# Kernel optimization log

Measured on AMD Instinct MI355X. Metric: run time of the kernel, lower is better.

The kernel has to match this reference:

```python
import jax, jax.numpy as jnp
import numpy as np

TAU = 2.0      # LIF membrane time constant
EPS = 1e-5     # BatchNorm eps
ALPHA = 4.0    # spikingjelly default Sigmoid surrogate alpha

@jax.custom_vjp
def spike(v):
    return (v >= 0.0).astype(v.dtype)

def _spike_fwd(v):
    return (v >= 0.0).astype(v.dtype), v

def _spike_bwd(v, g):
    s = jax.nn.sigmoid(ALPHA * v)
    return (g * ALPHA * s * (1.0 - s),)

spike.defvjp(_spike_fwd, _spike_bwd)

def lif(x_seq, v_th=1.0):
    # MultiStepLIFNode: v' = v + (x - v)/tau; spike = H(v' - v_th); hard reset to 0 (detach_reset)
    def step(v, x):
        v = v + (x - v) / TAU
        s = spike(v - v_th)
        v = v * (1.0 - jax.lax.stop_gradient(s))
        return v, s
    _, spikes = jax.lax.scan(step, jnp.zeros_like(x_seq[0]), x_seq)
    return spikes

def bn(y, gamma, beta, mean, var, trailing):
    # inference-mode BatchNorm over channel axis 2 of [T,B,C,...]
    shp = (1, 1, -1) + (1,) * trailing
    inv = gamma / jnp.sqrt(var + EPS)
    return (y - mean.reshape(shp)) * inv.reshape(shp) + beta.reshape(shp)

def setup_inputs() -> dict:
    T, B, C, H, W = 4, 32, 512, 16, 16
    key = jax.random.key(0)
    ks = jax.random.split(key, 12)
    return {
        "x": jax.random.normal(ks[0], (T, B, C, H, W), jnp.float32),
        "q_w": jax.random.normal(ks[1], (C, C), jnp.float32) * 0.02,
        "k_w": jax.random.normal(ks[2], (C, C), jnp.float32) * 0.02,
        "v_w": jax.random.normal(ks[3], (C, C), jnp.float32) * 0.02,
        "proj_w": jax.random.normal(ks[4], (C, C), jnp.float32) * 0.02,
        "proj_b": jax.random.normal(ks[5], (C,), jnp.float32) * 0.02,
        "dwc_w": jax.random.normal(ks[6], (C, 1, 5, 5), jnp.float32) * 0.1,
        "dwc_b": jax.random.normal(ks[7], (C,), jnp.float32) * 0.02,
        "bn_gamma": jax.random.uniform(ks[8], (5, C), jnp.float32, 0.5, 1.5),
        "bn_beta": jax.random.normal(ks[9], (5, C), jnp.float32) * 0.1,
        "bn_mean": jax.random.normal(ks[10], (5, C), jnp.float32) * 0.1,
        "bn_var": jax.random.uniform(ks[11], (5, C), jnp.float32, 0.5, 1.5),
    }

def reference(x, q_w, k_w, v_w, proj_w, proj_b, dwc_w, dwc_b,
              bn_gamma, bn_beta, bn_mean, bn_var):
    T, B, C, H, W = x.shape
    num_heads = 8
    d = C // num_heads
    N = H * W
    scale = 0.125
    identity = x

    xs = lif(x).reshape(T, B, C, N)  # spike input, flatten spatial

    def conv_bn(w, idx):
        # 1x1 Conv1d == channel matmul, then inference BN
        y = jnp.einsum('tbcn,dc->tbdn', xs, w)
        return bn(y, bn_gamma[idx], bn_beta[idx], bn_mean[idx], bn_var[idx], 1)

    def to_heads(s):  # [T,B,C,N] -> [T,B,h,N,d]
        return s.reshape(T, B, num_heads, d, N).transpose(0, 1, 2, 4, 3)

    q = to_heads(lif(conv_bn(q_w, 0)))
    k = to_heads(lif(conv_bn(k_w, 1)))
    v = to_heads(lif(conv_bn(v_w, 2)))

    kv = jnp.einsum('tbhnd,tbhne->tbhde', k, v)        # k^T @ v : [d,d] per head
    o = jnp.einsum('tbhnd,tbhde->tbhne', q, kv) * scale  # q @ (kv)
    o = o.transpose(0, 1, 2, 4, 3).reshape(T, B, C, N)

    o = lif(o, v_th=0.5)  # attn_lif with v_threshold=0.5

    y = jnp.einsum('tbcn,dc->tbdn', o, proj_w) + proj_b.reshape(1, 1, -1, 1)
    y = bn(y, bn_gamma[3], bn_beta[3], bn_mean[3], bn_var[3], 1)
    y = y.reshape(T, B, C, H, W)

    z = lif(y).reshape(T * B, C, H, W)
    z = jax.lax.conv_general_dilated(
        z, dwc_w, (1, 1), 'SAME',
        dimension_numbers=('NCHW', 'OIHW', 'NCHW'),
        feature_group_count=C) + dwc_b.reshape(1, -1, 1, 1)
    z = z.reshape(T, B, C, H, W)
    z = bn(z, bn_gamma[4], bn_beta[4], bn_mean[4], bn_var[4], 2)
    return z + identity
```

## Files before the change

### kernel.cpp

```cpp
#include <hip/hip_runtime.h>

#define TT 4
#define BB 32
#define CC 512
#define NN 256
#define DH 64

typedef unsigned char u8;
typedef unsigned short ushort_t;
typedef unsigned int uint_t;
typedef unsigned long long u64;

typedef short bf16x8 __attribute__((ext_vector_type(8)));
typedef float f32x4 __attribute__((ext_vector_type(4)));

typedef __attribute__((address_space(1))) const void gv_t;
typedef __attribute__((address_space(3))) void lv_t;

static __device__ __forceinline__ void gload16(const void* g, void* l){
  __builtin_amdgcn_global_load_lds((gv_t*)g, (lv_t*)l, 16, 0, 0);
}

static __device__ __forceinline__ unsigned int pack4(unsigned int w){
  return (w & 1u) | ((w >> 7) & 2u) | ((w >> 14) & 4u) | ((w >> 21) & 8u);
}
static __device__ __forceinline__ unsigned int f2bf(float f){
  unsigned int u = __float_as_uint(f);
  return (u + 0x7FFFu + ((u >> 16) & 1u)) >> 16;
}
static __device__ __forceinline__ float bf2f(unsigned int b){
  return __uint_as_float(b << 16);
}

__global__ __launch_bounds__(256) void k_prep(
    const float* __restrict__ qw, const float* __restrict__ kw,
    const float* __restrict__ vw, const float* __restrict__ pw,
    const float* __restrict__ bg, const float* __restrict__ bb,
    const float* __restrict__ bm, const float* __restrict__ bv,
    const float* __restrict__ pb,
    ushort_t* __restrict__ wsp, float* __restrict__ bn2)
{
  int bid = blockIdx.x;
  if (bid < 4096){
    int idx = bid*256 + threadIdx.x;
    int g   = idx >> 18;
    int rem = idx & 262143;
    const float* W = (g==0)? qw : (g==1)? kw : (g==2)? vw : pw;
    float wv = W[rem];
    unsigned int u1 = f2bf(wv);  float r1 = wv - bf2f(u1);
    unsigned int u2 = f2bf(r1);  float r2 = r1 - bf2f(u2);
    unsigned int u3 = f2bf(r2);
    size_t base = (size_t)g*3*262144 + rem;
    wsp[base            ] = (ushort_t)u1;
    wsp[base + 262144   ] = (ushort_t)u2;
    wsp[base + 2*262144 ] = (ushort_t)u3;
  } else {
    for (int i = threadIdx.x; i < 2048; i += 256){
      int g = i >> 9, d = i & 511;
      float inv = bg[g*512+d] / sqrtf(bv[g*512+d] + 1e-5f);
      float bt  = bb[g*512+d] - bm[g*512+d]*inv + ((g==3)? pb[d]*inv : 0.f);
      bn2[i*2+0] = inv;
      bn2[i*2+1] = bt;
    }
  }
}

__global__ __launch_bounds__(256) void k_lif_x(const float* __restrict__ x,
                                               u8* __restrict__ xs){
  const int PL = BB*CC*NN;
  int i = blockIdx.x*256 + threadIdx.x;
  float v = 0.f;
#pragma unroll
  for (int t=0;t<TT;++t){
    float xv = x[(size_t)t*PL + i];
    v = v + (xv - v)*0.5f;
    if (v >= 1.0f){ xs[(size_t)t*PL + i] = 1; v = 0.f; }
    else          { xs[(size_t)t*PL + i] = 0; }
  }
}

__global__ __launch_bounds__(256, 2) void k_gemm_mfma(
    const u8* __restrict__ act, const ushort_t* __restrict__ wsp,
    const float* __restrict__ bn2, u8* __restrict__ out,
    u8* __restrict__ out_qt, float vth)
{
  __shared__ __align__(16) ushort_t Alds[3][128][32];
  __shared__ __align__(16) ushort_t Blds[4][4][16][40];

  const int b  = blockIdx.y;
  const int d0 = (blockIdx.x >> 2) * 128;
  const int n0 = (blockIdx.x & 3) * 64;
  const int tid = threadIdx.x;
  const int l   = tid & 63;
  const int wvi = tid >> 6;

  f32x4 acc[2][4][4];
#pragma unroll
  for (int df=0; df<2; ++df)
#pragma unroll
    for (int nf=0; nf<4; ++nf)
#pragma unroll
      for (int t=0; t<4; ++t)
        acc[df][nf][t] = (f32x4){0.f,0.f,0.f,0.f};

  const int ts = tid >> 6;
  const int kp = (tid >> 2) & 15;
  const int nr = tid & 3;
  const int kq = kp >> 2, jj = kp & 3;

  for (int c0 = 0; c0 < CC; c0 += 32){
#pragma unroll
    for (int i=0; i<6; ++i){
      int id  = i*256 + tid;
      int s   = id >> 9;
      int rem = id & 511;
      int d   = rem >> 2, p = rem & 3;
      int g   = p ^ ((d + (d>>2)) & 3);
      const ushort_t* src = wsp + (size_t)s*262144 + (size_t)(d0+d)*512 + c0 + g*8;
      gload16(src, (ushort_t*)Alds + (size_t)id*8);
    }
    {
      const u8* sp = act + (((size_t)ts*BB + b)*CC + (c0 + kp*2))*NN + n0 + nr*16;
      uint4 r0 = *(const uint4*)sp;
      uint4 r1 = *(const uint4*)(sp + NN);
      uint_t wa[4] = {r0.x, r0.y, r0.z, r0.w};
      uint_t wb[4] = {r1.x, r1.y, r1.z, r1.w};
#pragma unroll
      for (int c4=0; c4<4; ++c4){
#pragma unroll
        for (int by=0; by<4; ++by){
          int i = c4*4 + by;
          uint_t b0 = (wa[c4] >> (8*by)) & 1u;
          uint_t b1 = (wb[c4] >> (8*by)) & 1u;
          uint_t hv = b0*0x3F80u + b1*0x3F800000u;
          *((uint_t*)&Blds[ts][nr][i][kq*8] + jj) = hv;
        }
      }
    }
    __syncthreads();

    bf16x8 Af[3][2];
#pragma unroll
    for (int s=0; s<3; ++s)
#pragma unroll
      for (int df=0; df<2; ++df){
        int row = wvi*32 + df*16 + (l&15);
        int pc  = (l>>4) ^ ((row + (row>>2)) & 3);
        Af[s][df] = *(const bf16x8*)&Alds[s][row][pc*8];
      }

#pragma unroll
    for (int nf=0; nf<4; ++nf){
      bf16x8 Bf[4];
#pragma unroll
      for (int t=0; t<4; ++t)
        Bf[t] = *(const bf16x8*)&Blds[t][nf][l&15][(l>>4)*8];
#pragma unroll
      for (int s=0; s<3; ++s)
#pragma unroll
        for (int df=0; df<2; ++df)
#pragma unroll
          for (int t=0; t<4; ++t)
            acc[df][nf][t] = __builtin_amdgcn_mfma_f32_16x16x32_bf16(
                Af[s][df], Bf[t], acc[df][nf][t], 0, 0, 0);
    }
    __syncthreads();
  }

  if (out_qt){
#pragma unroll
    for (int df=0; df<2; ++df){
      int dbase = d0 + wvi*32 + df*16 + ((l>>4)<<2);
      int h = dbase >> 6, dh = dbase & 63;
      float inv4[4], bt4[4];
#pragma unroll
      for (int r=0;r<4;++r){ inv4[r] = bn2[(dbase+r)*2]; bt4[r] = bn2[(dbase+r)*2+1]; }
#pragma unroll
      for (int nf=0; nf<4; ++nf){
        int n = n0 + nf*16 + (l&15);
        float vm0=0.f, vm1=0.f, vm2=0.f, vm3=0.f;
#pragma unroll
        for (int t=0; t<4; ++t){
          uchar4 sv;
          float y0 = acc[df][nf][t][0]*inv4[0] + bt4[0];
          vm0 = vm0 + (y0 - vm0)*0.5f; sv.x = (vm0 >= vth); if (sv.x) vm0 = 0.f;
          float y1 = acc[df][nf][t][1]*inv4[1] + bt4[1];
          vm1 = vm1 + (y1 - vm1)*0.5f; sv.y = (vm1 >= vth); if (sv.y) vm1 = 0.f;
          float y2 = acc[df][nf][t][2]*inv4[2] + bt4[2];
          vm2 = vm2 + (y2 - vm2)*0.5f; sv.z = (vm2 >= vth); if (sv.z) vm2 = 0.f;
          float y3 = acc[df][nf][t][3]*inv4[3] + bt4[3];
          vm3 = vm3 + (y3 - vm3)*0.5f; sv.w = (vm3 >= vth); if (sv.w) vm3 = 0.f;
          *(uchar4*)(out_qt + ((((size_t)t*BB + b)*8 + h)*256 + n)*64 + dh) = sv;
        }
      }
    }
  } else {
#pragma unroll
    for (int df=0; df<2; ++df){
#pragma unroll
      for (int r=0; r<4; ++r){
        int d = d0 + wvi*32 + df*16 + ((l>>4)<<2) + r;
        float inv = bn2[d*2+0], bt = bn2[d*2+1];
#pragma unroll
        for (int nf=0; nf<4; ++nf){
          int n = n0 + nf*16 + (l&15);
          float v = 0.f;
#pragma unroll
          for (int t=0; t<4; ++t){
            float y = acc[df][nf][t][r] * inv + bt;
            v = v + (y - v)*0.5f;
            u8 s = (v >= vth);
            out[(((size_t)t*BB + b)*CC + d)*NN + n] = s;
            if (s) v = 0.f;
          }
        }
      }
    }
  }
}

__global__ __launch_bounds__(256, 1) void k_attn(const u8* __restrict__ qt,
                                                 const u8* __restrict__ ks,
                                                 const u8* __restrict__ vs,
                                                 u8* __restrict__ os)
{
  const int h = blockIdx.x, b = blockIdx.y;
  __shared__ u64 Kb[64][5];
  __shared__ u64 Vb[64][5];
  __shared__ __align__(16) ushort_t kvbf[64][88];
  const int tid = threadIdx.x;
  const int l   = tid & 63;
  const int wvi = tid >> 6;

  f32x4 vm[4][4];
#pragma unroll
  for (int nf=0;nf<4;++nf)
#pragma unroll
    for (int ef=0;ef<4;++ef) vm[nf][ef] = (f32x4){0.f,0.f,0.f,0.f};

  for (int t=0;t<TT;++t){
    size_t base  = ((size_t)t*BB + b)*CC*NN + (size_t)h*DH*NN;
    const u8* qtb = qt + (((size_t)t*BB + b)*8 + h)*256*64;

    bf16x8 aq[4][2];
#pragma unroll
    for (int nf=0; nf<4; ++nf){
      int n = wvi*64 + nf*16 + (l&15);
#pragma unroll
      for (int kf=0; kf<2; ++kf){
        uint2 qu = *(const uint2*)(qtb + (size_t)n*64 + kf*32 + (l>>4)*8);
        union { uint_t u[4]; bf16x8 v; } cv;
        cv.u[0] = (qu.x & 1u)*0x3F80u + ((qu.x >> 8) & 1u)*0x3F800000u;
        cv.u[1] = ((qu.x >> 16) & 1u)*0x3F80u + ((qu.x >> 24) & 1u)*0x3F800000u;
        cv.u[2] = (qu.y & 1u)*0x3F80u + ((qu.y >> 8) & 1u)*0x3F800000u;
        cv.u[3] = ((qu.y >> 16) & 1u)*0x3F80u + ((qu.y >> 24) & 1u)*0x3F800000u;
        aq[nf][kf] = cv.v;
      }
    }

#pragma unroll
    for (int p=0;p<4;++p){
      int idx = p*256 + tid;
      int d = idx >> 4;
      int piece = idx & 15;
      uint4 ku = *(const uint4*)(ks + base + (size_t)d*NN + piece*16);
      uint4 vu = *(const uint4*)(vs + base + (size_t)d*NN + piece*16);
      unsigned int kp16 = pack4(ku.x) | (pack4(ku.y)<<4) | (pack4(ku.z)<<8) | (pack4(ku.w)<<12);
      unsigned int vp16 = pack4(vu.x) | (pack4(vu.y)<<4) | (pack4(vu.z)<<8) | (pack4(vu.w)<<12);
      ((ushort_t*)Kb)[d*20 + piece] = (ushort_t)kp16;
      ((ushort_t*)Vb)[d*20 + piece] = (ushort_t)vp16;
    }
    __syncthreads();

    {
      int dd0 = (tid >> 4)*4, ee0 = (tid & 15)*4;
      int cnt[4][4] = {};
#pragma unroll
      for (int wi=0; wi<4; ++wi){
        u64 kw[4], vw[4];
#pragma unroll
        for (int i=0;i<4;++i) kw[i] = Kb[dd0+i][wi];
#pragma unroll
        for (int j=0;j<4;++j) vw[j] = Vb[ee0+j][wi];
#pragma unroll
        for (int i=0;i<4;++i)
#pragma unroll
          for (int j=0;j<4;++j)
            cnt[i][j] += __popcll(kw[i] & vw[j]);
      }
#pragma unroll
      for (int i=0;i<4;++i)
#pragma unroll
        for (int j=0;j<4;++j)
          kvbf[ee0+j][dd0+i] = (ushort_t)(__float_as_uint((float)cnt[i][j]) >> 16);
    }
    __syncthreads();

    f32x4 acc[4][4];
#pragma unroll
    for (int nf=0;nf<4;++nf)
#pragma unroll
      for (int ef=0;ef<4;++ef) acc[nf][ef] = (f32x4){0.f,0.f,0.f,0.f};

#pragma unroll
    for (int ef=0; ef<4; ++ef){
      bf16x8 bv[2];
#pragma unroll
      for (int kf=0; kf<2; ++kf)
        bv[kf] = *(const bf16x8*)&kvbf[ef*16 + (l&15)][kf*32 + (l>>4)*8];
#pragma unroll
      for (int nf=0; nf<4; ++nf)
#pragma unroll
        for (int kf=0; kf<2; ++kf)
          acc[nf][ef] = __builtin_amdgcn_mfma_f32_16x16x32_bf16(
              aq[nf][kf], bv[kf], acc[nf][ef], 0, 0, 0);
    }

#pragma unroll
    for (int nf=0; nf<4; ++nf){
#pragma unroll
      for (int ef=0; ef<4; ++ef){
        int e = ef*16 + (l&15);
        int n4 = wvi*64 + nf*16 + ((l>>4)<<2);
        uchar4 sv;
        float o0 = acc[nf][ef][0]*0.125f;
        vm[nf][ef][0] += (o0 - vm[nf][ef][0])*0.5f; sv.x = (vm[nf][ef][0] >= 0.5f); if (sv.x) vm[nf][ef][0] = 0.f;
        float o1 = acc[nf][ef][1]*0.125f;
        vm[nf][ef][1] += (o1 - vm[nf][ef][1])*0.5f; sv.y = (vm[nf][ef][1] >= 0.5f); if (sv.y) vm[nf][ef][1] = 0.f;
        float o2 = acc[nf][ef][2]*0.125f;
        vm[nf][ef][2] += (o2 - vm[nf][ef][2])*0.5f; sv.z = (vm[nf][ef][2] >= 0.5f); if (sv.z) vm[nf][ef][2] = 0.f;
        float o3 = acc[nf][ef][3]*0.125f;
        vm[nf][ef][3] += (o3 - vm[nf][ef][3])*0.5f; sv.w = (vm[nf][ef][3] >= 0.5f); if (sv.w) vm[nf][ef][3] = 0.f;
        *(uchar4*)(os + base + (size_t)e*NN + n4) = sv;
      }
    }
    __syncthreads();
  }
}

__global__ __launch_bounds__(256) void k_dwc(const u8* __restrict__ zs,
                                             const float* __restrict__ x,
                                             const float* __restrict__ dwc_w,
                                             const float* __restrict__ dwc_b,
                                             const float* __restrict__ g4,
                                             const float* __restrict__ b4,
                                             const float* __restrict__ m4,
                                             const float* __restrict__ v4,
                                             float* __restrict__ out)
{
  const int c = blockIdx.x, b = blockIdx.y, t = blockIdx.z;
  __shared__ float zp[20][20];
  __shared__ float wk[25];
  const int tid = threadIdx.x;
  size_t base = (((size_t)t*BB + b)*CC + c)*NN;

  for (int idx = tid; idx < 400; idx += 256){
    int yy = idx/20 - 2, xx = idx%20 - 2;
    float v = 0.f;
    if (yy >= 0 && yy < 16 && xx >= 0 && xx < 16) v = (float)zs[base + yy*16 + xx];
    zp[idx/20][idx%20] = v;
  }
  if (tid < 25) wk[tid] = dwc_w[c*25 + tid];
  __syncthreads();

  const int py = tid >> 4, px = tid & 15;
  float s = 0.f;
#pragma unroll
  for (int i=0;i<5;++i)
#pragma unroll
    for (int j=0;j<5;++j)
      s = fmaf(zp[py+i][px+j], wk[i*5+j], s);
  s += dwc_b[c];
  float inv = g4[c] / sqrtf(v4[c] + 1e-5f);
  float r = (s - m4[c])*inv + b4[c] + x[base + tid];
  out[base + tid] = r;
}

extern "C" void kernel_launch(void* const* d_in, const int* in_sizes, int n_in,
                              void* d_out, int out_size, void* d_ws, size_t ws_size,
                              hipStream_t stream) {
  const float* x      = (const float*)d_in[0];
  const float* q_w    = (const float*)d_in[1];
  const float* k_w    = (const float*)d_in[2];
  const float* v_w    = (const float*)d_in[3];
  const float* proj_w = (const float*)d_in[4];
  const float* proj_b = (const float*)d_in[5];
  const float* dwc_w  = (const float*)d_in[6];
  const float* dwc_b  = (const float*)d_in[7];
  const float* bn_g   = (const float*)d_in[8];
  const float* bn_b   = (const float*)d_in[9];
  const float* bn_m   = (const float*)d_in[10];
  const float* bn_v   = (const float*)d_in[11];
  float* out = (float*)d_out;

  const size_t SZ = (size_t)TT*BB*CC*NN;
  u8* xs  = (u8*)d_ws;
  u8* qtp = xs + SZ;
  u8* ks  = qtp + SZ;
  u8* vs  = ks + SZ;
  u8* os  = vs + SZ;
  u8* zsp = os + SZ;
  ushort_t* wsp = (ushort_t*)(zsp + SZ);
  float* bn2    = (float*)(wsp + (size_t)4*3*262144);

  k_prep<<<4097, 256, 0, stream>>>(q_w, k_w, v_w, proj_w,
      bn_g, bn_b, bn_m, bn_v, proj_b, wsp, bn2);

  k_lif_x<<<(BB*CC*NN)/256, 256, 0, stream>>>(x, xs);

  dim3 gg(16, BB);
  k_gemm_mfma<<<gg, 256, 0, stream>>>(xs, wsp + (size_t)0*3*262144, bn2 + 0*1024, nullptr, qtp, 1.0f);
  k_gemm_mfma<<<gg, 256, 0, stream>>>(xs, wsp + (size_t)1*3*262144, bn2 + 1*1024, ks, nullptr, 1.0f);
  k_gemm_mfma<<<gg, 256, 0, stream>>>(xs, wsp + (size_t)2*3*262144, bn2 + 2*1024, vs, nullptr, 1.0f);

  k_attn<<<dim3(8, BB), 256, 0, stream>>>(qtp, ks, vs, os);

  k_gemm_mfma<<<gg, 256, 0, stream>>>(os, wsp + (size_t)3*3*262144, bn2 + 3*1024, zsp, nullptr, 1.0f);

  k_dwc<<<dim3(CC, BB, TT), 256, 0, stream>>>(zsp, x, dwc_w, dwc_b,
      bn_g + 4*CC, bn_b + 4*CC, bn_m + 4*CC, bn_v + 4*CC, out);
}
```

Measured before the change: 408.5 us.

## Use two-term fp16 weight split, vectorize LIF, and register-tile depthwise conv

```diff
diff --git a/kernel.cpp b/kernel.cpp
--- a/kernel.cpp
+++ b/kernel.cpp
@@ -1,4 +1,5 @@
 #include <hip/hip_runtime.h>
+#include <hip/hip_fp16.h>
 
 #define TT 4
 #define BB 32
@@ -11,7 +12,8 @@
 typedef unsigned int uint_t;
 typedef unsigned long long u64;
 
-typedef short bf16x8 __attribute__((ext_vector_type(8)));
+typedef _Float16 f16;
+typedef _Float16 f16x8 __attribute__((ext_vector_type(8)));
 typedef float f32x4 __attribute__((ext_vector_type(4)));
 
 typedef __attribute__((address_space(1))) const void gv_t;
@@ -23,13 +25,6 @@
 
 static __device__ __forceinline__ unsigned int pack4(unsigned int w){
   return (w & 1u) | ((w >> 7) & 2u) | ((w >> 14) & 4u) | ((w >> 21) & 8u);
-}
-static __device__ __forceinline__ unsigned int f2bf(float f){
-  unsigned int u = __float_as_uint(f);
-  return (u + 0x7FFFu + ((u >> 16) & 1u)) >> 16;
-}
-static __device__ __forceinline__ float bf2f(unsigned int b){
-  return __uint_as_float(b << 16);
 }
 
 __global__ __launch_bounds__(256) void k_prep(
@@ -37,7 +32,7 @@
     const float* __restrict__ vw, const float* __restrict__ pw,
     const float* __restrict__ bg, const float* __restrict__ bb,
     const float* __restrict__ bm, const float* __restrict__ bv,
-    const float* __restrict__ pb,
+    const float* __restrict__ pb, const float* __restrict__ dwcb,
     ushort_t* __restrict__ wsp, float* __restrict__ bn2)
 {
   int bid = blockIdx.x;
@@ -47,18 +42,18 @@
     int rem = idx & 262143;
     const float* W = (g==0)? qw : (g==1)? kw : (g==2)? vw : pw;
     float wv = W[rem];
-    unsigned int u1 = f2bf(wv);  float r1 = wv - bf2f(u1);
-    unsigned int u2 = f2bf(r1);  float r2 = r1 - bf2f(u2);
-    unsigned int u3 = f2bf(r2);
-    size_t base = (size_t)g*3*262144 + rem;
-    wsp[base            ] = (ushort_t)u1;
-    wsp[base + 262144   ] = (ushort_t)u2;
-    wsp[base + 2*262144 ] = (ushort_t)u3;
+    __half h1 = __float2half(wv);
+    float h1f = __half2float(h1);
+    __half h2 = __float2half((wv - h1f) * 2048.0f);
+    size_t base = (size_t)g*2*262144 + rem;
+    wsp[base         ] = __half_as_ushort(h1);
+    wsp[base + 262144] = __half_as_ushort(h2);
   } else {
-    for (int i = threadIdx.x; i < 2048; i += 256){
+    for (int i = threadIdx.x; i < 2560; i += 256){
       int g = i >> 9, d = i & 511;
-      float inv = bg[g*512+d] / sqrtf(bv[g*512+d] + 1e-5f);
-      float bt  = bb[g*512+d] - bm[g*512+d]*inv + ((g==3)? pb[d]*inv : 0.f);
+      float inv = bg[i] / sqrtf(bv[i] + 1e-5f);
+      float extra = (g==3)? pb[d] : (g==4)? dwcb[d] : 0.f;
+      float bt  = bb[i] - bm[i]*inv + extra*inv;
       bn2[i*2+0] = inv;
       bn2[i*2+1] = bt;
     }
@@ -68,14 +63,17 @@
 __global__ __launch_bounds__(256) void k_lif_x(const float* __restrict__ x,
                                                u8* __restrict__ xs){
   const int PL = BB*CC*NN;
-  int i = blockIdx.x*256 + threadIdx.x;
-  float v = 0.f;
+  int i = (blockIdx.x*256 + threadIdx.x)*4;
+  float4 v = make_float4(0.f,0.f,0.f,0.f);
 #pragma unroll
   for (int t=0;t<TT;++t){
-    float xv = x[(size_t)t*PL + i];
-    v = v + (xv - v)*0.5f;
-    if (v >= 1.0f){ xs[(size_t)t*PL + i] = 1; v = 0.f; }
-    else          { xs[(size_t)t*PL + i] = 0; }
+    float4 xv = *(const float4*)(x + (size_t)t*PL + i);
+    uchar4 s;
+    v.x = v.x + (xv.x - v.x)*0.5f; s.x = (v.x >= 1.0f); if (s.x) v.x = 0.f;
+    v.y = v.y + (xv.y - v.y)*0.5f; s.y = (v.y >= 1.0f); if (s.y) v.y = 0.f;
+    v.z = v.z + (xv.z - v.z)*0.5f; s.z = (v.z >= 1.0f); if (s.z) v.z = 0.f;
+    v.w = v.w + (xv.w - v.w)*0.5f; s.w = (v.w >= 1.0f); if (s.w) v.w = 0.f;
+    *(uchar4*)(xs + (size_t)t*PL + i) = s;
   }
 }
 
@@ -84,7 +82,7 @@
     const float* __restrict__ bn2, u8* __restrict__ out,
     u8* __restrict__ out_qt, float vth)
 {
-  __shared__ __align__(16) ushort_t Alds[3][128][32];
+  __shared__ __align__(16) ushort_t Alds[2][128][32];
   __shared__ __align__(16) ushort_t Blds[4][4][16][40];
 
   const int b  = blockIdx.y;
@@ -108,9 +106,11 @@
   const int nr = tid & 3;
   const int kq = kp >> 2, jj = kp & 3;
 
+  const f16 sc = (f16)4.8828125e-4f;
+
   for (int c0 = 0; c0 < CC; c0 += 32){
 #pragma unroll
-    for (int i=0; i<6; ++i){
+    for (int i=0; i<4; ++i){
       int id  = i*256 + tid;
       int s   = id >> 9;
       int rem = id & 511;
@@ -132,37 +132,44 @@
           int i = c4*4 + by;
           uint_t b0 = (wa[c4] >> (8*by)) & 1u;
           uint_t b1 = (wb[c4] >> (8*by)) & 1u;
-          uint_t hv = b0*0x3F80u + b1*0x3F800000u;
+          uint_t hv = b0*0x3C00u + b1*0x3C000000u;
           *((uint_t*)&Blds[ts][nr][i][kq*8] + jj) = hv;
         }
       }
     }
     __syncthreads();
 
-    bf16x8 Af[3][2];
-#pragma unroll
-    for (int s=0; s<3; ++s)
+    f16x8 Af[2][2];
+#pragma unroll
+    for (int s=0; s<2; ++s)
 #pragma unroll
       for (int df=0; df<2; ++df){
         int row = wvi*32 + df*16 + (l&15);
         int pc  = (l>>4) ^ ((row + (row>>2)) & 3);
-        Af[s][df] = *(const bf16x8*)&Alds[s][row][pc*8];
+        Af[s][df] = *(const f16x8*)&Alds[s][row][pc*8];
       }
 
 #pragma unroll
     for (int nf=0; nf<4; ++nf){
-      bf16x8 Bf[4];
+      f16x8 Bf[4];
 #pragma unroll
       for (int t=0; t<4; ++t)
-        Bf[t] = *(const bf16x8*)&Blds[t][nf][l&15][(l>>4)*8];
-#pragma unroll
-      for (int s=0; s<3; ++s)
-#pragma unroll
-        for (int df=0; df<2; ++df)
-#pragma unroll
-          for (int t=0; t<4; ++t)
-            acc[df][nf][t] = __builtin_amdgcn_mfma_f32_16x16x32_bf16(
-                Af[s][df], Bf[t], acc[df][nf][t], 0, 0, 0);
+        Bf[t] = *(const f16x8*)&Blds[t][nf][l&15][(l>>4)*8];
+#pragma unroll
+      for (int df=0; df<2; ++df)
+#pragma unroll
+        for (int t=0; t<4; ++t)
+          acc[df][nf][t] = __builtin_amdgcn_mfma_f32_16x16x32_f16(
+              Af[0][df], Bf[t], acc[df][nf][t], 0, 0, 0);
+#pragma unroll
+      for (int t=0; t<4; ++t)
+        Bf[t] = Bf[t] * sc;
+#pragma unroll
+      for (int df=0; df<2; ++df)
+#pragma unroll
+        for (int t=0; t<4; ++t)
+          acc[df][nf][t] = __builtin_amdgcn_mfma_f32_16x16x32_f16(
+              Af[1][df], Bf[t], acc[df][nf][t], 0, 0, 0);
     }
     __syncthreads();
   }
@@ -231,6 +238,8 @@
   const int tid = threadIdx.x;
   const int l   = tid & 63;
   const int wvi = tid >> 6;
+
+  typedef short bf16x8 __attribute__((ext_vector_type(8)));
 
   f32x4 vm[4][4];
 #pragma unroll
@@ -341,39 +350,64 @@
 __global__ __launch_bounds__(256) void k_dwc(const u8* __restrict__ zs,
                                              const float* __restrict__ x,
                                              const float* __restrict__ dwc_w,
-                                             const float* __restrict__ dwc_b,
-                                             const float* __restrict__ g4,
-                                             const float* __restrict__ b4,
-                                             const float* __restrict__ m4,
-                                             const float* __restrict__ v4,
+                                             const float* __restrict__ bn2,
                                              float* __restrict__ out)
 {
-  const int c = blockIdx.x, b = blockIdx.y, t = blockIdx.z;
-  __shared__ float zp[20][20];
-  __shared__ float wk[25];
-  const int tid = threadIdx.x;
-  size_t base = (((size_t)t*BB + b)*CC + c)*NN;
-
-  for (int idx = tid; idx < 400; idx += 256){
-    int yy = idx/20 - 2, xx = idx%20 - 2;
-    float v = 0.f;
-    if (yy >= 0 && yy < 16 && xx >= 0 && xx < 16) v = (float)zs[base + yy*16 + xx];
-    zp[idx/20][idx%20] = v;
-  }
-  if (tid < 25) wk[tid] = dwc_w[c*25 + tid];
-  __syncthreads();
-
-  const int py = tid >> 4, px = tid & 15;
-  float s = 0.f;
-#pragma unroll
-  for (int i=0;i<5;++i)
-#pragma unroll
-    for (int j=0;j<5;++j)
-      s = fmaf(zp[py+i][px+j], wk[i*5+j], s);
-  s += dwc_b[c];
-  float inv = g4[c] / sqrtf(v4[c] + 1e-5f);
-  float r = (s - m4[c])*inv + b4[c] + x[base + tid];
-  out[base + tid] = r;
+  int idx   = blockIdx.x*256 + threadIdx.x;
+  int y     = idx & 15;
+  int plane = idx >> 4;
+  int c     = plane & (CC-1);
+  size_t base = (size_t)plane * NN;
+
+  uint4 rows[5];
+#pragma unroll
+  for (int i=0;i<5;++i){
+    int yy = y + i - 2;
+    rows[i] = (yy >= 0 && yy < 16) ? *(const uint4*)(zs + base + yy*16)
+                                   : make_uint4(0,0,0,0);
+  }
+  float4 xr[4];
+#pragma unroll
+  for (int q=0;q<4;++q) xr[q] = *(const float4*)(x + base + y*16 + q*4);
+
+  float wk[25];
+  const float* wp = dwc_w + c*25;
+#pragma unroll
+  for (int i=0;i<25;++i) wk[i] = wp[i];
+  float inv = bn2[(2048+c)*2+0], bt = bn2[(2048+c)*2+1];
+
+  float acc[16];
+#pragma unroll
+  for (int i=0;i<16;++i) acc[i] = 0.f;
+
+#pragma unroll
+  for (int i=0;i<5;++i){
+    float rb[20];
+    rb[0]=0.f; rb[1]=0.f; rb[18]=0.f; rb[19]=0.f;
+    uint_t wd[4] = {rows[i].x, rows[i].y, rows[i].z, rows[i].w};
+#pragma unroll
+    for (int q=0;q<4;++q)
+#pragma unroll
+      for (int k=0;k<4;++k)
+        rb[2 + q*4 + k] = (float)((wd[q] >> (8*k)) & 0xffu);
+#pragma unroll
+    for (int j=0;j<5;++j){
+      float wv = wk[i*5+j];
+#pragma unroll
+      for (int xp=0;xp<16;++xp)
+        acc[xp] = fmaf(wv, rb[xp+j], acc[xp]);
+    }
+  }
+
+#pragma unroll
+  for (int q=0;q<4;++q){
+    float4 ov;
+    ov.x = acc[q*4+0]*inv + bt + xr[q].x;
+    ov.y = acc[q*4+1]*inv + bt + xr[q].y;
+    ov.z = acc[q*4+2]*inv + bt + xr[q].z;
+    ov.w = acc[q*4+3]*inv + bt + xr[q].w;
+    *(float4*)(out + base + y*16 + q*4) = ov;
+  }
 }
 
 extern "C" void kernel_launch(void* const* d_in, const int* in_sizes, int n_in,
@@ -401,22 +435,21 @@
   u8* os  = vs + SZ;
   u8* zsp = os + SZ;
   ushort_t* wsp = (ushort_t*)(zsp + SZ);
-  float* bn2    = (float*)(wsp + (size_t)4*3*262144);
+  float* bn2    = (float*)(wsp + (size_t)4*2*262144);
 
   k_prep<<<4097, 256, 0, stream>>>(q_w, k_w, v_w, proj_w,
-      bn_g, bn_b, bn_m, bn_v, proj_b, wsp, bn2);
-
-  k_lif_x<<<(BB*CC*NN)/256, 256, 0, stream>>>(x, xs);
+      bn_g, bn_b, bn_m, bn_v, proj_b, dwc_b, wsp, bn2);
+
+  k_lif_x<<<(BB*CC*NN)/1024, 256, 0, stream>>>(x, xs);
 
   dim3 gg(16, BB);
-  k_gemm_mfma<<<gg, 256, 0, stream>>>(xs, wsp + (size_t)0*3*262144, bn2 + 0*1024, nullptr, qtp, 1.0f);
-  k_gemm_mfma<<<gg, 256, 0, stream>>>(xs, wsp + (size_t)1*3*262144, bn2 + 1*1024, ks, nullptr, 1.0f);
-  k_gemm_mfma<<<gg, 256, 0, stream>>>(xs, wsp + (size_t)2*3*262144, bn2 + 2*1024, vs, nullptr, 1.0f);
+  k_gemm_mfma<<<gg, 256, 0, stream>>>(xs, wsp + (size_t)0*2*262144, bn2 + 0*1024, nullptr, qtp, 1.0f);
+  k_gemm_mfma<<<gg, 256, 0, stream>>>(xs, wsp + (size_t)1*2*262144, bn2 + 1*1024, ks, nullptr, 1.0f);
+  k_gemm_mfma<<<gg, 256, 0, stream>>>(xs, wsp + (size_t)2*2*262144, bn2 + 2*1024, vs, nullptr, 1.0f);
 
   k_attn<<<dim3(8, BB), 256, 0, stream>>>(qtp, ks, vs, os);
 
-  k_gemm_mfma<<<gg, 256, 0, stream>>>(os, wsp + (size_t)3*3*262144, bn2 + 3*1024, zsp, nullptr, 1.0f);
-
-  k_dwc<<<dim3(CC, BB, TT), 256, 0, stream>>>(zsp, x, dwc_w, dwc_b,
-      bn_g + 4*CC, bn_b + 4*CC, bn_m + 4*CC, bn_v + 4*CC, out);
-}
+  k_gemm_mfma<<<gg, 256, 0, stream>>>(os, wsp + (size_t)3*2*262144, bn2 + 3*1024, zsp, nullptr, 1.0f);
+
+  k_dwc<<<(TT*BB*CC*16)/256, 256, 0, stream>>>(zsp, x, dwc_w, bn2, out);
+}
```

Result: faster. 356.5 us (-12.7%).
